# Performance work log

Measured on AMD Instinct MI355X. Metric: run time of the kernel, lower is better.

The kernel has to match this reference:

```python
import jax, jax.numpy as jnp
import numpy as np

TEMP = 34.0   # Dynamic_conv2d default temperature
EPS = 1e-5    # BatchNorm eps


def setup_inputs() -> dict:
    key = jax.random.key(0)
    ks = jax.random.split(key, 4)
    B, Cin, Cout, H, W, K = 8, 32, 16, 256, 256, 4
    hidden = int(Cin * 0.25) + 1  # attention2d hidden planes = 9
    return {
        "x": jax.random.normal(ks[0], (B, Cin, H, W), jnp.float32),
        "weight": jax.random.normal(ks[1], (K, Cout, Cin, 3, 3), jnp.float32) * 0.05,
        "bias": jnp.zeros((K, Cout), jnp.float32),
        "fc1_w": jax.random.normal(ks[2], (hidden, Cin), jnp.float32) * 0.1,
        "fc2_w": jax.random.normal(ks[3], (K, hidden), jnp.float32) * 0.1,
        "fc2_b": jnp.zeros((K,), jnp.float32),
        "bn_gamma": jnp.ones((Cout,), jnp.float32),
        "bn_beta": jnp.zeros((Cout,), jnp.float32),
        "bn_mean": jnp.zeros((Cout,), jnp.float32),
        "bn_var": jnp.ones((Cout,), jnp.float32),
    }


def reference(x, weight, bias, fc1_w, fc2_w, fc2_b, bn_gamma, bn_beta, bn_mean, bn_var):
    xu = jnp.repeat(jnp.repeat(x, 2, axis=2), 2, axis=3)  # [B, Cin, 2H, 2W]

    # 2) attention over K kernels: global avg pool -> 1x1 conv -> relu -> 1x1 conv -> softmax(logits/T)
    pooled = xu.mean(axis=(2, 3))                          # [B, Cin]
    h = jax.nn.relu(pooled @ fc1_w.T)                      # [B, hidden]
    logits = h @ fc2_w.T + fc2_b                           # [B, K]
    attn = jax.nn.softmax(logits / TEMP, axis=-1)          # [B, K]

    # 3) per-sample aggregated conv weights & bias (CondConv-style)
    agg_w = jnp.einsum('bk,koihw->boihw', attn, weight)    # [B, Cout, Cin, 3, 3]
    agg_b = attn @ bias                                    # [B, Cout]

    # 4) per-sample 3x3 conv, stride 1, padding 1 (vmap instead of grouped-conv trick)
    dn = jax.lax.conv_dimension_numbers((1,) + xu.shape[1:], agg_w.shape[1:],
                                        ('NCHW', 'OIHW', 'NCHW'))
    def conv_one(xi, wi, bi):
        y = jax.lax.conv_general_dilated(xi[None], wi, window_strides=(1, 1),
                                         padding=((1, 1), (1, 1)),
                                         dimension_numbers=dn)[0]
        return y + bi[:, None, None]
    y = jax.vmap(conv_one)(xu, agg_w, agg_b)               # [B, Cout, 2H, 2W]

    # 5) BatchNorm (inference with running stats) + ReLU
    scale = bn_gamma / jnp.sqrt(bn_var + EPS)
    shift = bn_beta - bn_mean * scale
    return jax.nn.relu(y * scale[:, None, None] + shift[:, None, None])
```

## Files before the change

### kernel.cpp

```cpp
#include <hip/hip_runtime.h>
#include <hip/hip_bf16.h>

#define B_  8
#define CIN 32
#define COUT 16
#define K_  4
#define HID 9
#define HIN 256
#define WIN 256
#define HW  (HIN * WIN)
#define HOUT 512
#define WOUT 512
#define TEMP 34.0f
#define EPS_ 1e-5f

#define SCOLS 36
#define SLAB  1232

typedef float f32x4 __attribute__((ext_vector_type(4)));
typedef __fp16 fp16x2 __attribute__((ext_vector_type(2)));
typedef __fp16 f16x8 __attribute__((ext_vector_type(8)));

union FragB { unsigned u[4]; f16x8 h; };

__device__ inline unsigned pk2(float a, float b) {
    union { fp16x2 f; unsigned u; } x;
    x.f = __builtin_amdgcn_cvt_pkrtz(a, b);
    return x.u;
}
__device__ inline unsigned short f16b(float v) {
    union { __fp16 h; unsigned short u; } x;
    x.h = (__fp16)v;
    return x.u;
}

__global__ __launch_bounds__(1024) void pool_kernel(const float* __restrict__ x,
                                                    float* __restrict__ pooled) {
    int bc = blockIdx.x;
    const float4* p = (const float4*)(x + (size_t)bc * HW);
    float s = 0.f;
    for (int i = threadIdx.x; i < HW / 4; i += 1024) {
        float4 v = p[i];
        s += v.x + v.y + v.z + v.w;
    }
    #pragma unroll
    for (int off = 32; off > 0; off >>= 1) s += __shfl_down(s, off);
    __shared__ float red[16];
    if ((threadIdx.x & 63) == 0) red[threadIdx.x >> 6] = s;
    __syncthreads();
    if (threadIdx.x < 16) {
        float t = red[threadIdx.x];
        t += __shfl_down(t, 8);
        t += __shfl_down(t, 4);
        t += __shfl_down(t, 2);
        t += __shfl_down(t, 1);
        if (threadIdx.x == 0) pooled[bc] = t * (1.f / HW);
    }
}

__global__ __launch_bounds__(256) void attn_weights_kernel(
    const float* __restrict__ pooled, const float* __restrict__ weight,
    const float* __restrict__ bias, const float* __restrict__ fc1_w,
    const float* __restrict__ fc2_w, const float* __restrict__ fc2_b,
    const float* __restrict__ gamma, const float* __restrict__ beta,
    const float* __restrict__ mean, const float* __restrict__ var,
    unsigned short* __restrict__ wpk16, float* __restrict__ bias_eff) {
    int b = blockIdx.x;
    __shared__ float attn[K_];
    if (threadIdx.x == 0) {
        const float* pb = pooled + b * CIN;
        float h[HID];
        for (int j = 0; j < HID; ++j) {
            float s = 0.f;
            for (int c = 0; c < CIN; ++c) s += pb[c] * fc1_w[j * CIN + c];
            h[j] = fmaxf(s, 0.f);
        }
        float lg[K_];
        float mx = -1e30f;
        for (int k = 0; k < K_; ++k) {
            float s = fc2_b[k];
            for (int j = 0; j < HID; ++j) s += h[j] * fc2_w[k * HID + j];
            lg[k] = s * (1.f / TEMP);
            mx = fmaxf(mx, lg[k]);
        }
        float den = 0.f;
        for (int k = 0; k < K_; ++k) { lg[k] = expf(lg[k] - mx); den += lg[k]; }
        for (int k = 0; k < K_; ++k) attn[k] = lg[k] / den;
    }
    __syncthreads();
    float a0 = attn[0], a1 = attn[1], a2 = attn[2], a3v = attn[3];

    for (int p = threadIdx.x; p < COUT * CIN; p += 256) {
        int o = p >> 5, i = p & 31;
        float scale = gamma[o] / sqrtf(var[o] + EPS_);
        const float* w0 = weight + ((size_t)(0 * COUT + o) * CIN + i) * 9;
        const int kstr = COUT * CIN * 9;
        float a3w[9];
        #pragma unroll
        for (int t = 0; t < 9; ++t)
            a3w[t] = scale * (a0 * w0[t] + a1 * w0[kstr + t] +
                              a2 * w0[2 * kstr + t] + a3v * w0[3 * kstr + t]);
        float tmp[2][2][3];
        #pragma unroll
        for (int kx = 0; kx < 3; ++kx) {
            tmp[0][0][kx] = a3w[0 * 3 + kx];
            tmp[0][1][kx] = a3w[1 * 3 + kx] + a3w[2 * 3 + kx];
            tmp[1][0][kx] = a3w[0 * 3 + kx] + a3w[1 * 3 + kx];
            tmp[1][1][kx] = a3w[2 * 3 + kx];
        }
        float w16[16];
        #pragma unroll
        for (int py = 0; py < 2; ++py)
            #pragma unroll
            for (int px = 0; px < 2; ++px)
                #pragma unroll
                for (int u = 0; u < 2; ++u)
                    #pragma unroll
                    for (int v = 0; v < 2; ++v) {
                        const float* t = tmp[py][u];
                        float val = (px == 0) ? (v == 0 ? t[0] : t[1] + t[2])
                                              : (v == 0 ? t[0] + t[1] : t[2]);
                        w16[(py * 2 + px) * 4 + u * 2 + v] = val;
                    }
        const int ks = i >> 3, g = (i >> 1) & 3, hf = i & 1;
        const int l = g * 16 + o;
        #pragma unroll
        for (int par = 0; par < 4; ++par)
            #pragma unroll
            for (int d = 0; d < 4; ++d)
                wpk16[(((size_t)(b * 16 + par * 4 + ks) * 64 + l) * 4 + d) * 2 +
                      hf] = f16b(w16[par * 4 + d]);
    }
    if (threadIdx.x < COUT) {
        int o = threadIdx.x;
        float scale = gamma[o] / sqrtf(var[o] + EPS_);
        float shift = beta[o] - mean[o] * scale;
        float s = a0 * bias[0 * COUT + o] + a1 * bias[1 * COUT + o] +
                  a2 * bias[2 * COUT + o] + a3v * bias[3 * COUT + o];
        bias_eff[b * COUT + o] = s * scale + shift;
    }
}

__global__ __launch_bounds__(256) void conv_kernel(
    const float* __restrict__ x, const unsigned* __restrict__ wpk,
    const float* __restrict__ bias_eff, float* __restrict__ out) {
    const int tile = blockIdx.x;
    const int b = blockIdx.y;
    const int r0 = (tile >> 3) * 32, c0 = (tile & 7) * 32;
    const int tid = threadIdx.x;

    __shared__ unsigned lds32[16 * SLAB];

    const int w = tid >> 6, lane = tid & 63;
    const int g = lane >> 4, n = lane & 15;

    const float* xb = x + (size_t)b * CIN * HW;

    #pragma unroll
    for (int i2 = 0; i2 < 16; ++i2) {
        const float* p0 = xb + (size_t)(2 * i2) * HW;
        #pragma unroll
        for (int t = 0; t < 3; ++t) {
            int u = tid + t * 256;
            bool live = u < 34 * 18;
            int pr = u / 18, j = u - pr * 18;
            int gr = r0 - 1 + pr;
            int gc0 = c0 - 2 + 2 * j;
            bool rok = live & ((unsigned)gr < (unsigned)HIN);
            int ro = min(max(gr, 0), HIN - 1) * WIN;
            int cc = min(max(gc0, 0), WIN - 2);
            const float* pa = p0 + ro + cc;
            float2 v0 = *(const float2*)pa;
            float2 v1 = *(const float2*)(pa + HW);
            bool ok0 = rok & ((unsigned)gc0 < (unsigned)WIN);
            bool ok1 = rok & ((unsigned)(gc0 + 1) < (unsigned)WIN);
            if (!ok0) { v0.x = 0.f; v1.x = 0.f; }
            if (!ok1) { v0.y = 0.f; v1.y = 0.f; }
            if (live) {
                uint2 st;
                st.x = pk2(v0.x, v1.x);
                st.y = pk2(v0.y, v1.y);
                *(uint2*)&lds32[i2 * SLAB + pr * SCOLS + 2 * j] = st;
            }
        }
    }

    f16x8 areg[4][4];
    {
        const f16x8* wp = (const f16x8*)wpk + (size_t)b * 1024 + lane;
        #pragma unroll
        for (int par = 0; par < 4; ++par)
            #pragma unroll
            for (int ks = 0; ks < 4; ++ks)
                areg[par][ks] = wp[(par * 4 + ks) * 64];
    }
    float bias4[4];
    #pragma unroll
    for (int q = 0; q < 4; ++q) bias4[q] = bias_eff[b * COUT + g * 4 + q];

    __syncthreads();

    for (int h = 0; h < 2; ++h) {
        #pragma unroll
        for (int p2 = 0; p2 < 4; ++p2) {
            const int rA = w * 8 + p2 * 2;

            f32x4 acc[2][4];
            #pragma unroll
            for (int rr = 0; rr < 2; ++rr)
                #pragma unroll
                for (int par = 0; par < 4; ++par)
                    acc[rr][par] = (f32x4){0.f, 0.f, 0.f, 0.f};

            #pragma unroll
            for (int ks = 0; ks < 4; ++ks) {
                const int base =
                    (ks * 4 + g) * SLAB + rA * SCOLS + (h << 4) + n + 1;
                unsigned nb[4][3];
                #pragma unroll
                for (int rr = 0; rr < 4; ++rr)
                    #pragma unroll
                    for (int dv = 0; dv < 3; ++dv)
                        nb[rr][dv] = lds32[base + rr * SCOLS + dv];
                #pragma unroll
                for (int rr = 0; rr < 2; ++rr)
                    #pragma unroll
                    for (int par = 0; par < 4; ++par) {
                        const int py = par >> 1, px = par & 1;
                        FragB bf;
                        bf.u[0] = nb[rr + py][px];
                        bf.u[1] = nb[rr + py][px + 1];
                        bf.u[2] = nb[rr + py + 1][px];
                        bf.u[3] = nb[rr + py + 1][px + 1];
                        acc[rr][par] = __builtin_amdgcn_mfma_f32_16x16x32_f16(
                            areg[par][ks], bf.h, acc[rr][par], 0, 0, 0);
                    }
            }

            #pragma unroll
            for (int rr = 0; rr < 2; ++rr) {
                #pragma unroll
                for (int py = 0; py < 2; ++py) {
                    const int y = 2 * (r0 + rA + rr) + py;
                    #pragma unroll
                    for (int q = 0; q < 4; ++q) {
                        float2 st;
                        st.x = fmaxf(acc[rr][2 * py + 0][q] + bias4[q], 0.f);
                        st.y = fmaxf(acc[rr][2 * py + 1][q] + bias4[q], 0.f);
                        *(float2*)&out[((size_t)(b * COUT + g * 4 + q) * HOUT +
                                        y) * WOUT +
                                       2 * (c0 + (h << 4) + n)] = st;
                    }
                }
            }
        }
    }
}

extern "C" void kernel_launch(void* const* d_in, const int* in_sizes, int n_in,
                              void* d_out, int out_size, void* d_ws, size_t ws_size,
                              hipStream_t stream) {
    const float* x      = (const float*)d_in[0];
    const float* weight = (const float*)d_in[1];
    const float* bias   = (const float*)d_in[2];
    const float* fc1_w  = (const float*)d_in[3];
    const float* fc2_w  = (const float*)d_in[4];
    const float* fc2_b  = (const float*)d_in[5];
    const float* bn_g   = (const float*)d_in[6];
    const float* bn_b   = (const float*)d_in[7];
    const float* bn_m   = (const float*)d_in[8];
    const float* bn_v   = (const float*)d_in[9];
    float* out = (float*)d_out;

    float* ws = (float*)d_ws;
    float*    pooled   = ws;
    float*    bias_eff = ws + 256;
    unsigned* wpk      = (unsigned*)(ws + 512);

    pool_kernel<<<dim3(B_ * CIN), dim3(1024), 0, stream>>>(x, pooled);
    attn_weights_kernel<<<dim3(B_), dim3(256), 0, stream>>>(
        pooled, weight, bias, fc1_w, fc2_w, fc2_b, bn_g, bn_b, bn_m, bn_v,
        (unsigned short*)wpk, bias_eff);
    conv_kernel<<<dim3(64, B_), dim3(256), 0, stream>>>(
        x, wpk, bias_eff, out);
}
```

Before: 83.46 us.

## Double-buffer conv input tiles so global loads overlap MFMA compute

The conv kernel now uses 512-thread blocks that each handle two adjacent 32x32 tiles with two LDS buffers. Global loads for the second tile are issued into registers before each compute pass and written to LDS afterwards, so load latency can hide behind the MFMA work. Each wave now computes 4 rows at once, reusing more neighbourhood loads per step, and the pool kernel's loop is fully unrolled. The costs are double the LDS (about 158KB per block), more registers for the prefetch buffers, and half as many blocks, all of which may cut occupancy.

New measurement: 98.12 us. 1.18x slower.

```diff
diff --git a/kernel.cpp b/kernel.cpp
--- a/kernel.cpp
+++ b/kernel.cpp
@@ -16,6 +16,7 @@
 
 #define SCOLS 36
 #define SLAB  1232
+#define UNITS 612
 
 typedef float f32x4 __attribute__((ext_vector_type(4)));
 typedef __fp16 fp16x2 __attribute__((ext_vector_type(2)));
@@ -39,8 +40,9 @@
     int bc = blockIdx.x;
     const float4* p = (const float4*)(x + (size_t)bc * HW);
     float s = 0.f;
-    for (int i = threadIdx.x; i < HW / 4; i += 1024) {
-        float4 v = p[i];
+    #pragma unroll
+    for (int k = 0; k < 16; ++k) {
+        float4 v = p[threadIdx.x + k * 1024];
         s += v.x + v.y + v.z + v.w;
     }
     #pragma unroll
@@ -141,35 +143,52 @@
     }
 }
 
-__global__ __launch_bounds__(256) void conv_kernel(
+__global__ __launch_bounds__(512, 2) void conv_kernel(
     const float* __restrict__ x, const unsigned* __restrict__ wpk,
     const float* __restrict__ bias_eff, float* __restrict__ out) {
-    const int tile = blockIdx.x;
+    const int kb = blockIdx.x;
     const int b = blockIdx.y;
-    const int r0 = (tile >> 3) * 32, c0 = (tile & 7) * 32;
+    const int tile_y = kb >> 2, tile_xp = kb & 3;
+    const int r0 = tile_y * 32;
+    const int c0A = tile_xp * 64, c0B = c0A + 32;
     const int tid = threadIdx.x;
 
-    __shared__ unsigned lds32[16 * SLAB];
+    __shared__ unsigned ldsA[16 * SLAB];
+    __shared__ unsigned ldsB[16 * SLAB];
 
     const int w = tid >> 6, lane = tid & 63;
     const int g = lane >> 4, n = lane & 15;
-
     const float* xb = x + (size_t)b * CIN * HW;
 
+    f16x8 areg[4][4];
+    {
+        const f16x8* wp = (const f16x8*)wpk + (size_t)b * 1024 + lane;
+        #pragma unroll
+        for (int par = 0; par < 4; ++par)
+            #pragma unroll
+            for (int ks = 0; ks < 4; ++ks)
+                areg[par][ks] = wp[(par * 4 + ks) * 64];
+    }
+    float bias4[4];
     #pragma unroll
-    for (int i2 = 0; i2 < 16; ++i2) {
-        const float* p0 = xb + (size_t)(2 * i2) * HW;
-        #pragma unroll
-        for (int t = 0; t < 3; ++t) {
-            int u = tid + t * 256;
-            bool live = u < 34 * 18;
-            int pr = u / 18, j = u - pr * 18;
+    for (int q = 0; q < 4; ++q) bias4[q] = bias_eff[b * COUT + g * 4 + q];
+
+    auto stage_inline = [&](unsigned* lds, int c0, int chunk) {
+        #pragma unroll
+        for (int t = 0; t < 10; ++t) {
+            int u = tid + t * 512;
+            bool live = u < 8 * UNITS;
+            int uu = live ? u : 0;
+            int s = uu / UNITS;
+            int r = uu - s * UNITS;
+            int pr = r / 18, j = r - pr * 18;
+            int slab = chunk * 8 + s;
             int gr = r0 - 1 + pr;
             int gc0 = c0 - 2 + 2 * j;
-            bool rok = live & ((unsigned)gr < (unsigned)HIN);
+            bool rok = (unsigned)gr < (unsigned)HIN;
             int ro = min(max(gr, 0), HIN - 1) * WIN;
             int cc = min(max(gc0, 0), WIN - 2);
-            const float* pa = p0 + ro + cc;
+            const float* pa = xb + (size_t)(2 * slab) * HW + ro + cc;
             float2 v0 = *(const float2*)pa;
             float2 v1 = *(const float2*)(pa + HW);
             bool ok0 = rok & ((unsigned)gc0 < (unsigned)WIN);
@@ -180,81 +199,120 @@
                 uint2 st;
                 st.x = pk2(v0.x, v1.x);
                 st.y = pk2(v0.y, v1.y);
-                *(uint2*)&lds32[i2 * SLAB + pr * SCOLS + 2 * j] = st;
+                *(uint2*)&lds[slab * SLAB + pr * SCOLS + 2 * j] = st;
             }
         }
-    }
-
-    f16x8 areg[4][4];
-    {
-        const f16x8* wp = (const f16x8*)wpk + (size_t)b * 1024 + lane;
-        #pragma unroll
-        for (int par = 0; par < 4; ++par)
-            #pragma unroll
-            for (int ks = 0; ks < 4; ++ks)
-                areg[par][ks] = wp[(par * 4 + ks) * 64];
-    }
-    float bias4[4];
-    #pragma unroll
-    for (int q = 0; q < 4; ++q) bias4[q] = bias_eff[b * COUT + g * 4 + q];
-
-    __syncthreads();
-
-    for (int h = 0; h < 2; ++h) {
-        #pragma unroll
-        for (int p2 = 0; p2 < 4; ++p2) {
-            const int rA = w * 8 + p2 * 2;
-
-            f32x4 acc[2][4];
-            #pragma unroll
-            for (int rr = 0; rr < 2; ++rr)
+    };
+
+    float2 Lv0[10], Lv1[10];
+    auto stage_issue = [&](int c0, int chunk) {
+        #pragma unroll
+        for (int t = 0; t < 10; ++t) {
+            int u = tid + t * 512;
+            int uu = (u < 8 * UNITS) ? u : 0;
+            int s = uu / UNITS;
+            int r = uu - s * UNITS;
+            int pr = r / 18, j = r - pr * 18;
+            int gr = r0 - 1 + pr;
+            int gc0 = c0 - 2 + 2 * j;
+            int ro = min(max(gr, 0), HIN - 1) * WIN;
+            int cc = min(max(gc0, 0), WIN - 2);
+            const float* pa = xb + (size_t)(2 * (chunk * 8 + s)) * HW + ro + cc;
+            Lv0[t] = *(const float2*)pa;
+            Lv1[t] = *(const float2*)(pa + HW);
+        }
+    };
+    auto stage_write = [&](unsigned* lds, int c0, int chunk) {
+        #pragma unroll
+        for (int t = 0; t < 10; ++t) {
+            int u = tid + t * 512;
+            bool live = u < 8 * UNITS;
+            int uu = live ? u : 0;
+            int s = uu / UNITS;
+            int r = uu - s * UNITS;
+            int pr = r / 18, j = r - pr * 18;
+            int gr = r0 - 1 + pr;
+            int gc0 = c0 - 2 + 2 * j;
+            bool rok = (unsigned)gr < (unsigned)HIN;
+            float2 v0 = Lv0[t], v1 = Lv1[t];
+            bool ok0 = rok & ((unsigned)gc0 < (unsigned)WIN);
+            bool ok1 = rok & ((unsigned)(gc0 + 1) < (unsigned)WIN);
+            if (!ok0) { v0.x = 0.f; v1.x = 0.f; }
+            if (!ok1) { v0.y = 0.f; v1.y = 0.f; }
+            if (live) {
+                uint2 st;
+                st.x = pk2(v0.x, v1.x);
+                st.y = pk2(v0.y, v1.y);
+                *(uint2*)&lds[(chunk * 8 + s) * SLAB + pr * SCOLS + 2 * j] = st;
+            }
+        }
+    };
+
+    auto compute_quad = [&](const unsigned* lds, int c0, int h) {
+        const int rA = w * 4;
+        f32x4 acc[4][4];
+        #pragma unroll
+        for (int rr = 0; rr < 4; ++rr)
+            #pragma unroll
+            for (int par = 0; par < 4; ++par)
+                acc[rr][par] = (f32x4){0.f, 0.f, 0.f, 0.f};
+
+        #pragma unroll
+        for (int ks = 0; ks < 4; ++ks) {
+            const int base =
+                (ks * 4 + g) * SLAB + rA * SCOLS + (h << 4) + n + 1;
+            unsigned nb[6][3];
+            #pragma unroll
+            for (int rr = 0; rr < 6; ++rr)
                 #pragma unroll
-                for (int par = 0; par < 4; ++par)
-                    acc[rr][par] = (f32x4){0.f, 0.f, 0.f, 0.f};
-
-            #pragma unroll
-            for (int ks = 0; ks < 4; ++ks) {
-                const int base =
-                    (ks * 4 + g) * SLAB + rA * SCOLS + (h << 4) + n + 1;
-                unsigned nb[4][3];
+                for (int dv = 0; dv < 3; ++dv)
+                    nb[rr][dv] = lds[base + rr * SCOLS + dv];
+            #pragma unroll
+            for (int rr = 0; rr < 4; ++rr)
                 #pragma unroll
-                for (int rr = 0; rr < 4; ++rr)
-                    #pragma unroll
-                    for (int dv = 0; dv < 3; ++dv)
-                        nb[rr][dv] = lds32[base + rr * SCOLS + dv];
+                for (int par = 0; par < 4; ++par) {
+                    const int py = par >> 1, px = par & 1;
+                    FragB bf;
+                    bf.u[0] = nb[rr + py][px];
+                    bf.u[1] = nb[rr + py][px + 1];
+                    bf.u[2] = nb[rr + py + 1][px];
+                    bf.u[3] = nb[rr + py + 1][px + 1];
+                    acc[rr][par] = __builtin_amdgcn_mfma_f32_16x16x32_f16(
+                        areg[par][ks], bf.h, acc[rr][par], 0, 0, 0);
+                }
+        }
+        #pragma unroll
+        for (int rr = 0; rr < 4; ++rr) {
+            #pragma unroll
+            for (int py = 0; py < 2; ++py) {
+                const int y = 2 * (r0 + rA + rr) + py;
                 #pragma unroll
-                for (int rr = 0; rr < 2; ++rr)
-                    #pragma unroll
-                    for (int par = 0; par < 4; ++par) {
-                        const int py = par >> 1, px = par & 1;
-                        FragB bf;
-                        bf.u[0] = nb[rr + py][px];
-                        bf.u[1] = nb[rr + py][px + 1];
-                        bf.u[2] = nb[rr + py + 1][px];
-                        bf.u[3] = nb[rr + py + 1][px + 1];
-                        acc[rr][par] = __builtin_amdgcn_mfma_f32_16x16x32_f16(
-                            areg[par][ks], bf.h, acc[rr][par], 0, 0, 0);
-                    }
-            }
-
-            #pragma unroll
-            for (int rr = 0; rr < 2; ++rr) {
-                #pragma unroll
-                for (int py = 0; py < 2; ++py) {
-                    const int y = 2 * (r0 + rA + rr) + py;
-                    #pragma unroll
-                    for (int q = 0; q < 4; ++q) {
-                        float2 st;
-                        st.x = fmaxf(acc[rr][2 * py + 0][q] + bias4[q], 0.f);
-                        st.y = fmaxf(acc[rr][2 * py + 1][q] + bias4[q], 0.f);
-                        *(float2*)&out[((size_t)(b * COUT + g * 4 + q) * HOUT +
-                                        y) * WOUT +
-                                       2 * (c0 + (h << 4) + n)] = st;
-                    }
+                for (int q = 0; q < 4; ++q) {
+                    float2 st;
+                    st.x = fmaxf(acc[rr][2 * py + 0][q] + bias4[q], 0.f);
+                    st.y = fmaxf(acc[rr][2 * py + 1][q] + bias4[q], 0.f);
+                    *(float2*)&out[((size_t)(b * COUT + g * 4 + q) * HOUT + y) *
+                                       WOUT +
+                                   2 * (c0 + (h << 4) + n)] = st;
                 }
             }
         }
-    }
+    };
+
+    stage_inline(ldsA, c0A, 0);
+    stage_inline(ldsA, c0A, 1);
+    __syncthreads();
+
+    stage_issue(c0B, 0);
+    compute_quad(ldsA, c0A, 0);
+    stage_write(ldsB, c0B, 0);
+    stage_issue(c0B, 1);
+    compute_quad(ldsA, c0A, 1);
+    stage_write(ldsB, c0B, 1);
+    __syncthreads();
+
+    compute_quad(ldsB, c0B, 0);
+    compute_quad(ldsB, c0B, 1);
 }
 
 extern "C" void kernel_launch(void* const* d_in, const int* in_sizes, int n_in,
@@ -281,6 +339,6 @@
     attn_weights_kernel<<<dim3(B_), dim3(256), 0, stream>>>(
         pooled, weight, bias, fc1_w, fc2_w, fc2_b, bn_g, bn_b, bn_m, bn_v,
         (unsigned short*)wpk, bias_eff);
-    conv_kernel<<<dim3(64, B_), dim3(256), 0, stream>>>(
+    conv_kernel<<<dim3(32, B_), dim3(512), 0, stream>>>(
         x, wpk, bias_eff, out);
 }
```
